# Kernel tuning notes

Hardware: AMD Instinct MI355X
Metric: run time of the kernel (lower is better)

The kernel has to match this reference:

```python
import jax, jax.numpy as jnp
import numpy as np

B, C, K, V, S = 16384, 1024, 128, 256, 6
HM, HG, M = 512, 384, 1024
LB = 2
GATE_DIM = C + K + 2 * V + 5  # 1669
CADENCE = 8.0
TEMP = 0.25
REFRESH_T, SPAWN_T, PROMOTE_T, RETIRE_T = 0.55, 0.60, 0.50, 0.15
DECAY = 0.995
EPS_N = 1e-6


def _mlp(x, W1, b1, W2, b2):
    return jax.nn.gelu(x @ W1 + b1, approximate=False) @ W2 + b2


def _l2norm(x):
    n = jnp.linalg.norm(x, axis=-1, keepdims=True)
    return x / jnp.maximum(n, EPS_N)


def setup_inputs():
    key = jax.random.key(0)
    ks = jax.random.split(key, 16)
    p = lambda k, sh: (0.02 * jax.random.normal(k, sh)).astype(jnp.float32)
    return {
        "context": jax.random.normal(ks[0], (B, C), jnp.float32),
        "ledger_bias": jax.random.normal(ks[1], (B, LB), jnp.float32),
        "keys": jax.random.normal(ks[2], (B, S, K), jnp.float32),
        "values": jax.random.normal(ks[3], (B, S, V), jnp.float32),
        "confidence": jax.random.uniform(ks[4], (B, S, 1), jnp.float32),
        "age": 16.0 * jax.random.uniform(ks[5], (B, S, 1), jnp.float32),
        "alive": (jax.random.uniform(ks[6], (B, S, 1)) > 0.3).astype(jnp.float32),
        "Wk1": p(ks[7], (C, HM)), "bk1": jnp.zeros(HM, jnp.float32),
        "Wk2": p(ks[8], (HM, K)), "bk2": jnp.zeros(K, jnp.float32),
        "Wv1": p(ks[9], (C, HM)), "bv1": jnp.zeros(HM, jnp.float32),
        "Wv2": p(ks[10], (HM, V)), "bv2": jnp.zeros(V, jnp.float32),
        "Wg1": p(ks[11], (4, GATE_DIM, HG)), "bg1": jnp.zeros((4, HG), jnp.float32),
        "Wg2": p(ks[12], (4, HG, 1)), "bg2": jnp.zeros((4, 1), jnp.float32),
        "Wsum": p(ks[13], (V, M)), "bsum": jnp.zeros(M, jnp.float32),
        "g_ln": jnp.ones(M, jnp.float32), "b_ln": jnp.zeros(M, jnp.float32),
    }


def _forward(context, ledger_bias, keys, values, confidence, age, alive,
             Wk1, bk1, Wk2, bk2, Wv1, bv1, Wv2, bv2,
             Wg1, bg1, Wg2, bg2, Wsum, bsum, g_ln, b_ln):
    cand_key = _l2norm(_mlp(context, Wk1, bk1, Wk2, bk2))   # [B,K]
    cand_val = _mlp(context, Wv1, bv1, Wv2, bv2)            # [B,V]
    # --- slot match: cosine similarity over live slots, gather best ---
    live = alive[..., 0] > 0                                # [B,S]
    safe_keys = _l2norm(keys + (1.0 - alive) * 1e-4)
    scores = jnp.einsum("bd,bsd->bs", cand_key, safe_keys)
    scores = jnp.where(live, scores, -1e4)
    has_live = jnp.any(live, axis=1, keepdims=True)         # [B,1]
    best_score = jnp.where(has_live, scores.max(axis=1, keepdims=True), 0.0)
    best_index = jnp.where(has_live, jnp.argmax(scores, axis=1, keepdims=True), 0)
    matched_val = jnp.take_along_axis(values, best_index[:, :, None], axis=1)[:, 0]
    matched_age = jnp.take_along_axis(age, best_index[:, :, None], axis=1)[:, 0]
    cadence_prior = jax.nn.sigmoid((matched_age - CADENCE) / CADENCE)
    surprise = 1.0 - best_score
    feats = jnp.concatenate([context, cand_key, cand_val, matched_val,
                             best_score, cadence_prior, surprise, ledger_bias], axis=-1)
    # --- four gate MLPs fused into one batched einsum ---
    h = jax.nn.gelu(jnp.einsum("bf,gfh->bgh", feats, Wg1) + bg1, approximate=False)
    probs = jax.nn.sigmoid(jnp.einsum("bgh,gho->bgo", h, Wg2) + bg2)[:, :, 0]  # [B,4]
    refresh_p, spawn_p, promote_p, retire_p = (probs[:, i:i + 1] for i in range(4))
    # --- soft masks (hard=False path) ---
    has_live_f = alive.max(axis=1)                          # [B,1]
    t = max(TEMP, 1e-4)
    refresh_raw = jax.nn.sigmoid((refresh_p - REFRESH_T) / t) * has_live_f
    spawn_raw = jax.nn.sigmoid((spawn_p - SPAWN_T) / t)
    denom = 1.0 + refresh_raw + spawn_raw
    refresh = refresh_raw / denom
    spawn = spawn_raw / denom
    promote = jax.nn.sigmoid((promote_p - PROMOTE_T) / t)
    retire = jax.nn.sigmoid((retire_p - RETIRE_T) / t)
    # --- spawn slot selection ---
    inactive = (alive[..., 0] < 0.5).astype(jnp.float32)
    has_inactive = inactive.max(axis=1, keepdims=True) > 0.5
    inactive_choice = jnp.argmax(inactive, axis=1, keepdims=True)
    utility = (confidence - 0.01 * age)[..., 0]
    utility = jnp.where(best_index == jnp.arange(S)[None, :], 1e4, utility)
    spawn_index = jnp.where(has_inactive, inactive_choice,
                            jnp.argmin(utility, axis=1, keepdims=True))
    # --- masked scatter update into slot memory ---
    match_hot = jax.nn.one_hot(best_index[:, 0], S, dtype=keys.dtype)[:, :, None]
    spawn_hot = jax.nn.one_hot(spawn_index[:, 0], S, dtype=keys.dtype)[:, :, None]
    refresh_slot = match_hot * refresh[:, None, :]
    spawn_slot = spawn_hot * spawn[:, None, :]
    retire_slot = match_hot * retire[:, None, :]
    write = jnp.clip(refresh_slot + spawn_slot, 0.0, 1.0)
    keys_n = keys * (1.0 - write) + write * cand_key[:, None, :]
    values_n = values * (1.0 - write) + write * cand_val[:, None, :]
    conf_n = (confidence * DECAY * (1.0 - write) + write) * (1.0 - retire_slot)
    age_n = (age + alive) * (1.0 - write)
    alive_n = jnp.clip(alive * (1.0 - retire_slot) + write, 0.0, 1.0)
    # --- confidence-weighted summary + promoted memory token ---
    w = alive_n * conf_n
    summary = (values_n * w).sum(axis=1) / (w.sum(axis=1) + EPS_N)  # [B,V]
    z = summary @ Wsum + bsum
    mu = z.mean(axis=-1, keepdims=True)
    var = ((z - mu) ** 2).mean(axis=-1, keepdims=True)
    promoted = promote * (((z - mu) / jnp.sqrt(var + 1e-5)) * g_ln + b_ln)
    return promoted, summary, keys_n, values_n, conf_n, age_n, alive_n


def reference(context, ledger_bias, keys, values, confidence, age, alive,
              Wk1, bk1, Wk2, bk2, Wv1, bv1, Wv2, bv2,
              Wg1, bg1, Wg2, bg2, Wsum, bsum, g_ln, b_ln):
    return _forward(context, ledger_bias, keys, values, confidence, age, alive,
                    Wk1, bk1, Wk2, bk2, Wv1, bv1, Wv2, bv2,
                    Wg1, bg1, Wg2, bg2, Wsum, bsum, g_ln, b_ln)
```

## Files before the change

### kernel.cpp

```cpp
#include <hip/hip_runtime.h>
#include <math.h>

static constexpr int Bsz  = 16384;
static constexpr int Cdim = 1024;
static constexpr int Kdim = 128;
static constexpr int Vdim = 256;
static constexpr int HMd  = 512;
static constexpr int GOUTd= 1536;
static constexpr int GDIM = 1669;
static constexpr int GPAD = 1728;
static constexpr int F2D  = 704;
static constexpr int Mdim = 1024;
static constexpr float TAU = 2e-3f;

typedef __attribute__((ext_vector_type(8))) _Float16 f16x8;
typedef __attribute__((ext_vector_type(4))) float f32x4;

__device__ __forceinline__ float sigm(float x){ return 1.0f/(1.0f+expf(-x)); }
__device__ __forceinline__ float gelu(float x){ return 0.5f*x*(1.0f+erff(x*0.70710678118654752440f)); }
__device__ __forceinline__ ushort f2h(float f){
    return __builtin_bit_cast(ushort, (_Float16)f);
}


__global__ __launch_bounds__(256) void k_zero(int* p){ if (threadIdx.x==0) *p = 0; }

__global__ __launch_bounds__(256) void k_cat(float* __restrict__ dst,
        const float* __restrict__ a, const float* __restrict__ b, int na, int ntot){
    int i = blockIdx.x*256 + threadIdx.x;
    if (i >= ntot) return;
    dst[i] = (i < na) ? a[i] : b[i-na];
}

__global__ __launch_bounds__(256) void k_wt(const float* __restrict__ W,
                                            ushort* __restrict__ Wt, int K, int N){
    __shared__ float tile[64][65];
    int n0 = blockIdx.x*64, k0 = blockIdx.y*64;
    int tx = threadIdx.x & 63, ty = threadIdx.x >> 6;
    #pragma unroll
    for (int i=0;i<64;i+=4)
        tile[ty+i][tx] = W[(size_t)(k0+ty+i)*N + n0 + tx];
    __syncthreads();
    #pragma unroll
    for (int i=0;i<64;i+=4)
        Wt[(size_t)(n0+ty+i)*K + k0 + tx] = f2h(tile[tx][ty+i]);
}

__global__ __launch_bounds__(256) void k_wg1t(const float* __restrict__ Wg1,
                                              ushort* __restrict__ Wt){
    __shared__ float tile[64][65];
    int g = blockIdx.z;
    int h0 = blockIdx.x*64, f0 = blockIdx.y*64;
    int tx = threadIdx.x & 63, ty = threadIdx.x >> 6;
    #pragma unroll
    for (int i=0;i<64;i+=4){
        int f = f0+ty+i;
        tile[ty+i][tx] = (f < GDIM) ? Wg1[((size_t)g*GDIM+f)*384 + h0+tx] : 0.0f;
    }
    __syncthreads();
    #pragma unroll
    for (int i=0;i<64;i+=4)
        Wt[((size_t)(g*384 + h0+ty+i))*GPAD + f0+tx] = f2h(tile[tx][ty+i]);
}

__global__ __launch_bounds__(256) void k_cvt(const float* __restrict__ x,
                                             ushort* __restrict__ y, size_t n4){
    size_t i = (size_t)blockIdx.x*256 + threadIdx.x;
    if (i >= n4) return;
    float4 v = ((const float4*)x)[i];
    ushort4 o = { f2h(v.x), f2h(v.y), f2h(v.z), f2h(v.w) };
    ((ushort4*)y)[i] = o;
}

__device__ __forceinline__ void gload_lds16(const void* g, void* l){
    typedef __attribute__((address_space(1))) const unsigned gu32;
    typedef __attribute__((address_space(3))) unsigned lu32;
    __builtin_amdgcn_global_load_lds((gu32*)(unsigned long long)g,
                                     (lu32*)(unsigned)(unsigned long long)l,
                                     16, 0, 0);
}

template<int ACT, int OUTM, int SRC, int NX>
__global__ __launch_bounds__(256) void k_mgemm(const ushort* __restrict__ A,
        const ushort* __restrict__ A2, const ushort* __restrict__ Bt,
        const float* __restrict__ bias, const float* __restrict__ Wg2,
        void* __restrict__ Cout, int K, int lda){
    __shared__ alignas(16) ushort lds[16384];
    ushort* As = lds;
    ushort* Bs = lds + 8192;
    int t = threadIdx.x;
    int l = t & 63, w = t >> 6;
    int wm = w >> 1, wn = w & 1;
    int nwg = NX * (int)gridDim.y;
    int orig = (int)blockIdx.y * NX + (int)blockIdx.x;
    int qq = nwg >> 3, rr = nwg & 7;
    int xcd = orig & 7, loc = orig >> 3;
    int wgid = (xcd < rr ? xcd*(qq+1) : rr*(qq+1) + (xcd-rr)*qq) + loc;
    int bx = wgid % NX;
    int by = wgid / NX;
    size_t row0 = (size_t)by * 128;
    int col0 = bx * 128;
    constexpr int N = NX*128;
    f32x4 acc[4][4] = {};
    int lrow = l >> 3;
    int lc8  = (l & 7) ^ lrow;

    for (int k0 = 0; k0 < K; k0 += 64){
        const ushort* Ag; int astr, koff;
        if (SRC == 1){
            if (k0 < 1024){ Ag = A;  astr = 1024; koff = k0; }
            else          { Ag = A2; astr = F2D;  koff = k0 - 1024; }
        } else if (SRC == 2){
            Ag = A; astr = lda; koff = k0 + (bx ? 512 : 0);
        } else { Ag = A; astr = lda; koff = k0; }
        #pragma unroll
        for (int i = 0; i < 4; ++i){
            int ch = w*4 + i;
            int r  = ch*8 + lrow;
            gload_lds16(Ag + (row0 + r)*(size_t)astr + koff + lc8*8, As + ch*512);
            gload_lds16(Bt + (size_t)(col0 + r)*K + k0 + lc8*8, Bs + ch*512);
        }
        __syncthreads();
        #pragma unroll
        for (int kk = 0; kk < 2; ++kk){
            f16x8 af[4], bfr[4];
            int j8 = kk*4 + (l >> 4);
            #pragma unroll
            for (int m = 0; m < 4; ++m){
                int row = wm*64 + m*16 + (l & 15);
                int c16 = j8 ^ (row & 7);
                af[m] = *(const f16x8*)(const void*)(As + row*64 + c16*8);
            }
            #pragma unroll
            for (int n = 0; n < 4; ++n){
                int rowb = wn*64 + n*16 + (l & 15);
                int c16 = j8 ^ (rowb & 7);
                bfr[n] = *(const f16x8*)(const void*)(Bs + rowb*64 + c16*8);
            }
            #pragma unroll
            for (int m = 0; m < 4; ++m)
                #pragma unroll
                for (int n = 0; n < 4; ++n)
                    acc[m][n] = __builtin_amdgcn_mfma_f32_16x16x32_f16(af[m], bfr[n], acc[m][n], 0, 0, 0);
        }
        __syncthreads();
    }
    int q = l >> 4, cf = l & 15;
    if (OUTM == 2){
        float* sacc = (float*)lds;
        if (t < 128) sacc[t] = 0.f;
        __syncthreads();
        #pragma unroll
        for (int m = 0; m < 4; ++m){
            #pragma unroll
            for (int i = 0; i < 4; ++i){
                float v = 0.f;
                #pragma unroll
                for (int n = 0; n < 4; ++n){
                    int col = col0 + wn*64 + n*16 + cf;
                    float z = acc[m][n][i] + bias[col];
                    v += gelu(z) * Wg2[col];
                }
                atomicAdd(&sacc[wm*64 + m*16 + q*4 + i], v);
            }
        }
        __syncthreads();
        if (t < 128) ((float*)Cout)[(row0 + t)*NX + bx] = sacc[t];
    } else {
        #pragma unroll
        for (int m = 0; m < 4; ++m){
            #pragma unroll
            for (int n = 0; n < 4; ++n){
                int col = col0 + wn*64 + n*16 + cf;
                float bv = bias[col];
                #pragma unroll
                for (int i = 0; i < 4; ++i){
                    size_t r = row0 + wm*64 + m*16 + q*4 + i;
                    float v = acc[m][n][i] + bv;
                    if (ACT == 1) v = gelu(v);
                    if (OUTM == 1) ((ushort*)Cout)[r*N + col] = f2h(v);
                    else           ((float*) Cout)[r*N + col] = v;
                }
            }
        }
    }
}

template<int ACT>
__global__ __launch_bounds__(256) void k_gemm_dyn(const float* __restrict__ A,
                                                  const float* __restrict__ W,
                                                  const float* __restrict__ bias,
                                                  float* __restrict__ C,
                                                  const int* __restrict__ cntp,
                                                  int N, int K){
    int M = (*cntp + 63) & ~63;
    size_t row0 = (size_t)blockIdx.y * 64;
    if ((int)row0 >= M) return;
    __shared__ float As[32][68];
    __shared__ float Ws[32][64];
    int t  = threadIdx.x;
    int tx = t & 15, ty = t >> 4;
    int col0 = blockIdx.x * 64;
    float acc[4][4] = {};
    int ra = t >> 3;
    int ca = (t & 7) << 2;
    int rw = t >> 4;
    int cw = (t & 15) << 2;
    for (int k0 = 0; k0 < K; k0 += 32){
        float4 a0 = *(const float4*)(A + (row0 + ra)*K + k0 + ca);
        float4 a1 = *(const float4*)(A + (row0 + ra + 32)*K + k0 + ca);
        float4 w0 = *(const float4*)(W + (size_t)(k0 + rw)*N + col0 + cw);
        float4 w1 = *(const float4*)(W + (size_t)(k0 + rw + 16)*N + col0 + cw);
        As[ca+0][ra] = a0.x; As[ca+1][ra] = a0.y; As[ca+2][ra] = a0.z; As[ca+3][ra] = a0.w;
        As[ca+0][ra+32] = a1.x; As[ca+1][ra+32] = a1.y; As[ca+2][ra+32] = a1.z; As[ca+3][ra+32] = a1.w;
        *(float4*)&Ws[rw][cw]    = w0;
        *(float4*)&Ws[rw+16][cw] = w1;
        __syncthreads();
        #pragma unroll
        for (int kk = 0; kk < 32; ++kk){
            float4 av = *(const float4*)&As[kk][ty*4];
            float4 wv = *(const float4*)&Ws[kk][tx*4];
            float a4[4] = {av.x, av.y, av.z, av.w};
            float w4[4] = {wv.x, wv.y, wv.z, wv.w};
            #pragma unroll
            for (int i=0;i<4;i++)
                #pragma unroll
                for (int j=0;j<4;j++)
                    acc[i][j] = fmaf(a4[i], w4[j], acc[i][j]);
        }
        __syncthreads();
    }
    #pragma unroll
    for (int i=0;i<4;i++){
        size_t r = row0 + ty*4 + i;
        #pragma unroll
        for (int j=0;j<4;j++){
            int c = col0 + tx*4 + j;
            float v = acc[i][j] + bias[c];
            if (ACT == 1) v = gelu(v);
            C[r*N + c] = v;
        }
    }
}

__global__ __launch_bounds__(256) void k_gather(const float* __restrict__ ctx,
        const int* __restrict__ flaglist, const int* __restrict__ flagcnt,
        float* __restrict__ fctx, int b0){
    int i = (blockIdx.x<<2) + (threadIdx.x>>6);
    int lane = threadIdx.x & 63;
    int cnt = *flagcnt;
    int cntpad = (cnt + 63) & ~63;
    if (i >= cntpad) return;
    float4* dst = (float4*)(fctx + (size_t)i*1024);
    if (i < cnt){
        const float4* src = (const float4*)(ctx + ((size_t)b0 + flaglist[i])*1024);
        #pragma unroll
        for (int j=0;j<4;j++) dst[lane + 64*j] = src[lane + 64*j];
    } else {
        float4 z = {0.f,0.f,0.f,0.f};
        #pragma unroll
        for (int j=0;j<4;j++) dst[lane + 64*j] = z;
    }
}

__global__ __launch_bounds__(256) void k_fixapply(const float* __restrict__ fck,
        const float* __restrict__ keys, const float* __restrict__ values,
        const float* __restrict__ age,  const float* __restrict__ alive,
        float* __restrict__ ckc, ushort* __restrict__ feats2, int* __restrict__ bidx,
        const int* __restrict__ flagcnt, const int* __restrict__ flaglist, int b0){
    int i = (blockIdx.x<<2) + (threadIdx.x>>6);
    int lane = threadIdx.x & 63;
    if (i >= *flagcnt) return;
    int w = flaglist[i];
    size_t b = (size_t)b0 + w;
    float2 c2 = ((const float2*)(fck + (size_t)i*128))[lane];
    float ss = c2.x*c2.x + c2.y*c2.y;
    #pragma unroll
    for (int o=32;o;o>>=1) ss += __shfl_xor(ss,o);
    float inv = 1.0f / fmaxf(sqrtf(ss), 1e-6f);
    float2 cc; cc.x = c2.x*inv; cc.y = c2.y*inv;
    ((float2*)(ckc + (size_t)w*128))[lane] = cc;
    ushort* f2 = feats2 + (size_t)w*F2D;
    { ushort2 o = { f2h(cc.x), f2h(cc.y) };
      ((ushort2*)f2)[lane] = o; }
    float s1v = -1e30f; int bi = 0; int anylive = 0;
    #pragma unroll
    for (int s=0;s<6;s++){
        float a = alive[b*6+s];
        float2 k2 = ((const float2*)(keys + (b*6+s)*128))[lane];
        float ks = k2.x*k2.x + k2.y*k2.y;
        float dt = cc.x*k2.x + cc.y*k2.y;
        #pragma unroll
        for (int o=32;o;o>>=1){ ks += __shfl_xor(ks,o); dt += __shfl_xor(dt,o); }
        float sc;
        if (a > 0.0f){ sc = dt / fmaxf(sqrtf(ks), 1e-6f); anylive = 1; }
        else sc = -1e4f;
        if (sc > s1v){ s1v = sc; bi = s; }
    }
    int bis = anylive ? bi : 0;
    float bsc = anylive ? s1v : 0.0f;
    float4 mv = ((const float4*)(values + (b*6+bis)*256))[lane];
    ushort4 mo = { f2h(mv.x), f2h(mv.y), f2h(mv.z), f2h(mv.w) };
    ((ushort4*)(f2+384))[lane] = mo;
    if (lane == 0){
        bidx[w] = bis;
        float mage = age[b*6 + bis];
        f2[640] = f2h(bsc);
        f2[641] = f2h(sigm((mage - 8.0f)*0.125f));
        f2[642] = f2h(1.0f - bsc);
    }
}

__global__ __launch_bounds__(256) void k_feats(
        const float* __restrict__ ledger, const float* __restrict__ keys,
        const float* __restrict__ values, const float* __restrict__ age,
        const float* __restrict__ alive,  const float* __restrict__ ckv,
        float* __restrict__ ckc, ushort* __restrict__ feats2,
        int* __restrict__ bidx, int* __restrict__ flagcnt, int* __restrict__ flaglist,
        int b0){
    int w = (blockIdx.x<<2) + (threadIdx.x>>6);
    int lane = threadIdx.x & 63;
    size_t b = (size_t)b0 + w;
    const float* ckr = ckv + (size_t)w*384;
    float2 cr2 = ((const float2*)ckr)[lane];
    float ssc = cr2.x*cr2.x + cr2.y*cr2.y;
    #pragma unroll
    for (int o=32;o;o>>=1) ssc += __shfl_xor(ssc,o);
    float invc = 1.0f / fmaxf(sqrtf(ssc), 1e-6f);
    float2 cc; cc.x = cr2.x*invc; cc.y = cr2.y*invc;
    ((float2*)(ckc + (size_t)w*128))[lane] = cc;
    float s1v = -1e30f, s2v = -1e30f; int bi = 0; int anylive = 0;
    #pragma unroll
    for (int s=0;s<6;s++){
        float a = alive[b*6+s];
        float2 k2 = ((const float2*)(keys + (b*6+s)*128))[lane];
        float ss = k2.x*k2.x + k2.y*k2.y;
        float dt = cc.x*k2.x + cc.y*k2.y;
        #pragma unroll
        for (int o=32;o;o>>=1){ ss += __shfl_xor(ss,o); dt += __shfl_xor(dt,o); }
        float sc;
        if (a > 0.0f){ sc = dt / fmaxf(sqrtf(ss), 1e-6f); anylive = 1; }
        else sc = -1e4f;
        if (sc > s1v){ s2v = s1v; s1v = sc; bi = s; }
        else if (sc > s2v) s2v = sc;
    }
    float best_score = anylive ? s1v : 0.0f;
    int bis = anylive ? bi : 0;
    if (lane == 0 && (s1v - s2v) < TAU){
        int pos = atomicAdd(flagcnt, 1);
        flaglist[pos] = w;
    }
    float4 mv = ((const float4*)(values + (b*6+bis)*256))[lane];
    float mage = age[b*6+bis];
    float cad = sigm((mage - 8.0f)*0.125f);
    ushort* f2 = feats2 + (size_t)w*F2D;
    { ushort2 o = { f2h(cc.x), f2h(cc.y) };
      ((ushort2*)f2)[lane] = o; }
    { float4 v = ((const float4*)(ckr+128))[lane];
      ushort4 o = { f2h(v.x), f2h(v.y), f2h(v.z), f2h(v.w) };
      ((ushort4*)(f2+128))[lane] = o; }
    { ushort4 o = { f2h(mv.x), f2h(mv.y), f2h(mv.z), f2h(mv.w) };
      ((ushort4*)(f2+384))[lane] = o; }
    if (lane == 0){
        f2[640] = f2h(best_score);
        f2[641] = f2h(cad);
        f2[642] = f2h(1.0f - best_score);
        f2[643] = f2h(ledger[b*2]);
        f2[644] = f2h(ledger[b*2+1]);
        bidx[w] = bis;
    }
    if (lane < GPAD - GDIM) f2[645+lane] = 0;
}

__global__ __launch_bounds__(256) void k_update(const float* __restrict__ keys,
        const float* __restrict__ values, const float* __restrict__ conf,
        const float* __restrict__ age,    const float* __restrict__ alive,
        const float* __restrict__ ckC,    const float* __restrict__ ckv,
        const float* __restrict__ part,   const float* __restrict__ bg2,
        const int* __restrict__ bidx,
        float* __restrict__ probsC,
        float* __restrict__ o_keys, float* __restrict__ o_vals,
        float* __restrict__ o_conf, float* __restrict__ o_age,
        float* __restrict__ o_aliv, float* __restrict__ o_sum,
        ushort* __restrict__ o_sumb, int b0){
    int w = (blockIdx.x<<2) + (threadIdx.x>>6);
    int lane = threadIdx.x & 63;
    size_t b = (size_t)b0 + w;
    const float* pp = part + (size_t)w*12;
    float pb[4];
    #pragma unroll
    for (int g=0; g<4; ++g)
        pb[g] = sigm(pp[3*g] + pp[3*g+1] + pp[3*g+2] + bg2[g]);
    if (lane < 4) probsC[w*4 + lane] = pb[lane];
    float rp = pb[0], sp = pb[1], tp = pb[3];
    float al[6], cf[6], ag[6];
    float hl = 0.f;
    #pragma unroll
    for (int s=0;s<6;s++){
        al[s]=alive[b*6+s]; cf[s]=conf[b*6+s]; ag[s]=age[b*6+s];
        hl = fmaxf(hl, al[s]);
    }
    float rr = hl * sigm((rp-0.55f)*4.0f);
    float sr = sigm((sp-0.60f)*4.0f);
    float den = 1.0f + rr + sr;
    float refresh = rr/den, spawn = sr/den;
    float retire = sigm((tp-0.15f)*4.0f);
    int bi = bidx[w];
    int ic = -1;
    #pragma unroll
    for (int s=5;s>=0;s--) if (al[s] < 0.5f) ic = s;
    int si;
    if (ic >= 0) si = ic;
    else {
        float bu = 1e30f; int am = 0;
        #pragma unroll
        for (int s=0;s<6;s++){
            float u = (s == bi) ? 1e4f : (cf[s] - 0.01f*ag[s]);
            if (u < bu){ bu = u; am = s; }
        }
        si = am;
    }
    float2 cc  = ((const float2*)(ckC + (size_t)w*128))[lane];
    float4 cvv = ((const float4*)(ckv + (size_t)w*384 + 128))[lane];
    float s0=0,s1=0,s2=0,s3=0, wsum=0;
    #pragma unroll
    for (int s=0;s<6;s++){
        float wr = refresh*(s==bi ? 1.0f:0.0f) + spawn*(s==si ? 1.0f:0.0f);
        wr = fminf(wr, 1.0f);
        float rs = (s==bi) ? retire : 0.0f;
        float om = 1.0f - wr;
        float2 k2 = ((const float2*)(keys + (b*6+s)*128))[lane];
        float2 kn; kn.x = k2.x*om + wr*cc.x; kn.y = k2.y*om + wr*cc.y;
        ((float2*)(o_keys + (b*6+s)*128))[lane] = kn;
        float4 vv = ((const float4*)(values + (b*6+s)*256))[lane];
        float4 vn;
        vn.x = vv.x*om + wr*cvv.x; vn.y = vv.y*om + wr*cvv.y;
        vn.z = vv.z*om + wr*cvv.z; vn.w = vv.w*om + wr*cvv.w;
        ((float4*)(o_vals + (b*6+s)*256))[lane] = vn;
        float cn  = (cf[s]*0.995f*om + wr) * (1.0f - rs);
        float an  = fminf(fmaxf(al[s]*(1.0f - rs) + wr, 0.0f), 1.0f);
        float agn = (ag[s] + al[s]) * om;
        float wgt = an * cn;
        wsum += wgt;
        s0 += vn.x*wgt; s1 += vn.y*wgt; s2 += vn.z*wgt; s3 += vn.w*wgt;
        if (lane == s){ o_conf[b*6+s] = cn; o_age[b*6+s] = agn; o_aliv[b*6+s] = an; }
    }
    float inv = 1.0f/(wsum + 1e-6f);
    float4 sm; sm.x = s0*inv; sm.y = s1*inv; sm.z = s2*inv; sm.w = s3*inv;
    ((float4*)(o_sum + b*256))[lane] = sm;
    ushort4 sb = { f2h(sm.x), f2h(sm.y), f2h(sm.z), f2h(sm.w) };
    ((ushort4*)(o_sumb + (size_t)w*256))[lane] = sb;
}

__global__ __launch_bounds__(256) void k_ln(const float* __restrict__ z,
        const float* __restrict__ probs, const float* __restrict__ g_ln,
        const float* __restrict__ b_ln,  float* __restrict__ o_prom, int b0){
    int w = blockIdx.x; int t = threadIdx.x;
    int lane = t & 63, wid = t >> 6;
    float4 v = ((const float4*)(z + (size_t)w*1024))[t];
    float s = v.x+v.y+v.z+v.w;
    #pragma unroll
    for (int o=32;o;o>>=1) s += __shfl_xor(s,o);
    __shared__ float red[4];
    if (lane==0) red[wid] = s;
    __syncthreads();
    float mu = (red[0]+red[1]+red[2]+red[3]) * (1.0f/1024.0f);
    float d0=v.x-mu, d1=v.y-mu, d2=v.z-mu, d3=v.w-mu;
    float ss = d0*d0+d1*d1+d2*d2+d3*d3;
    #pragma unroll
    for (int o=32;o;o>>=1) ss += __shfl_xor(ss,o);
    __syncthreads();
    if (lane==0) red[wid] = ss;
    __syncthreads();
    float var = (red[0]+red[1]+red[2]+red[3]) * (1.0f/1024.0f);
    float rstd = 1.0f / sqrtf(var + 1e-5f);
    float pm = sigm((probs[w*4+2]-0.50f)*4.0f);
    float4 g  = ((const float4*)g_ln)[t];
    float4 bb = ((const float4*)b_ln)[t];
    float4 o;
    o.x = pm*(d0*rstd*g.x + bb.x);
    o.y = pm*(d1*rstd*g.y + bb.y);
    o.z = pm*(d2*rstd*g.z + bb.z);
    o.w = pm*(d3*rstd*g.w + bb.w);
    ((float4*)(o_prom + ((size_t)b0 + w)*1024))[t] = o;
}

extern "C" void kernel_launch(void* const* d_in, const int* in_sizes, int n_in,
                              void* d_out, int out_size, void* d_ws, size_t ws_size,
                              hipStream_t stream){
    const float* ctx    = (const float*)d_in[0];
    const float* ledger = (const float*)d_in[1];
    const float* keys   = (const float*)d_in[2];
    const float* values = (const float*)d_in[3];
    const float* conf   = (const float*)d_in[4];
    const float* age    = (const float*)d_in[5];
    const float* alive  = (const float*)d_in[6];
    const float* Wk1 = (const float*)d_in[7];  const float* bk1 = (const float*)d_in[8];
    const float* Wk2 = (const float*)d_in[9];  const float* bk2 = (const float*)d_in[10];
    const float* Wv1 = (const float*)d_in[11]; const float* bv1 = (const float*)d_in[12];
    const float* Wv2 = (const float*)d_in[13]; const float* bv2 = (const float*)d_in[14];
    const float* Wg1 = (const float*)d_in[15]; const float* bg1 = (const float*)d_in[16];
    const float* Wg2 = (const float*)d_in[17]; const float* bg2 = (const float*)d_in[18];
    const float* Wsum= (const float*)d_in[19]; const float* bsum= (const float*)d_in[20];
    const float* g_ln= (const float*)d_in[21]; const float* b_ln= (const float*)d_in[22];

    float* out   = (float*)d_out;
    float* o_prom= out;
    float* o_sum = o_prom + (size_t)Bsz*Mdim;
    float* o_keys= o_sum  + (size_t)Bsz*Vdim;
    float* o_vals= o_keys + (size_t)Bsz*6*Kdim;
    float* o_conf= o_vals + (size_t)Bsz*6*Vdim;
    float* o_age = o_conf + (size_t)Bsz*6;
    float* o_aliv= o_age  + (size_t)Bsz*6;

    char* p = (char*)d_ws;
    auto alloc = [&](size_t bytes)->char*{
        char* r = p; p += (bytes + 255) & ~(size_t)255; return r;
    };
    ushort* ctxh  = (ushort*)alloc((size_t)Bsz*Cdim*2);
    ushort* W1m   = (ushort*)alloc((size_t)1024*Cdim*2);
    ushort* W2m   = (ushort*)alloc((size_t)384*HMd*2);
    ushort* Wg1tt = (ushort*)alloc((size_t)GOUTd*GPAD*2);
    ushort* Wsumt = (ushort*)alloc((size_t)Mdim*Vdim*2);
    float*  biasm1= (float*) alloc(1024*4);
    float*  biasm2= (float*) alloc(384*4);
    size_t fixed = (size_t)(p - (char*)d_ws);
    size_t per_row = 2048  + 1536  + 512  + 1408
                   + 48  + 4096  + 512  + 16
                   + 4 + 4 + 2048  + 512  + 128 ;
    int CB = 16384;
    while (CB > 128 && fixed + (size_t)CB*per_row + 16384 > ws_size) CB >>= 1;
    ushort* H      = (ushort*)alloc((size_t)CB*1024*2);
    float*  ckv    = (float*) alloc((size_t)CB*384*4);
    float*  ckc    = (float*) alloc((size_t)CB*Kdim*4);
    ushort* feats2 = (ushort*)alloc((size_t)CB*F2D*2);
    float*  part   = (float*) alloc((size_t)CB*12*4);
    float*  zbuf   = (float*) alloc((size_t)CB*Mdim*4);
    ushort* sumb   = (ushort*)alloc((size_t)CB*Vdim*2);
    float*  probsC = (float*) alloc((size_t)CB*4*4);
    int*    bidxC  = (int*)   alloc((size_t)CB*4);
    int*    flagl  = (int*)   alloc((size_t)CB*4);
    int*    flagc  = (int*)   alloc(256);
    float*  fH     = (float*) alloc((size_t)CB*HMd*4);
    float*  fck    = (float*) alloc((size_t)CB*Kdim*4);
    float*  fctx   = zbuf;

    dim3 blk(256);
    k_cvt<<<(int)(((size_t)Bsz*Cdim/4 + 255)/256), blk, 0, stream>>>(ctx, ctxh, (size_t)Bsz*Cdim/4);
    k_wt<<<dim3(HMd/64,  Cdim/64), blk, 0, stream>>>(Wk1, W1m,             Cdim, HMd);
    k_wt<<<dim3(HMd/64,  Cdim/64), blk, 0, stream>>>(Wv1, W1m + 512*Cdim,  Cdim, HMd);
    k_wt<<<dim3(Kdim/64, HMd/64),  blk, 0, stream>>>(Wk2, W2m,             HMd, Kdim);
    k_wt<<<dim3(Vdim/64, HMd/64),  blk, 0, stream>>>(Wv2, W2m + 128*HMd,   HMd, Vdim);
    k_wt<<<dim3(Mdim/64, Vdim/64), blk, 0, stream>>>(Wsum, Wsumt, Vdim, Mdim);
    k_wg1t<<<dim3(384/64, GPAD/64, 4), blk, 0, stream>>>(Wg1, Wg1tt);
    k_cat<<<(1024+255)/256, blk, 0, stream>>>(biasm1, bk1, bv1, 512, 1024);
    k_cat<<<(384+255)/256,  blk, 0, stream>>>(biasm2, bk2, bv2, 128, 384);

    for (int b0 = 0; b0 < Bsz; b0 += CB){
        k_zero<<<1, blk, 0, stream>>>(flagc);
        k_mgemm<1,1,0,8><<<dim3(8, CB/128), blk, 0, stream>>>(
            ctxh + (size_t)b0*Cdim, nullptr, W1m, biasm1, nullptr, H, Cdim, Cdim);
        k_mgemm<0,0,2,3><<<dim3(3, CB/128), blk, 0, stream>>>(
            H, nullptr, W2m, biasm2, nullptr, ckv, HMd, 1024);
        k_feats<<<CB/4, blk, 0, stream>>>(ledger, keys, values, age, alive,
                                          ckv, ckc, feats2, bidxC, flagc, flagl, b0);
        k_gather<<<CB/4, blk, 0, stream>>>(ctx, flagl, flagc, fctx, b0);
        k_gemm_dyn<1><<<dim3(HMd/64,  CB/64), blk, 0, stream>>>(fctx, Wk1, bk1, fH,  flagc, HMd,  Cdim);
        k_gemm_dyn<0><<<dim3(Kdim/64, CB/64), blk, 0, stream>>>(fH,   Wk2, bk2, fck, flagc, Kdim, HMd);
        k_fixapply<<<CB/4, blk, 0, stream>>>(fck, keys, values, age, alive,
                                             ckc, feats2, bidxC, flagc, flagl, b0);
        k_mgemm<0,2,1,12><<<dim3(12, CB/128), blk, 0, stream>>>(
            ctxh + (size_t)b0*Cdim, feats2, Wg1tt, bg1, Wg2, part, GPAD, 0);
        k_update<<<CB/4, blk, 0, stream>>>(keys, values, conf, age, alive, ckc, ckv,
                                           part, bg2, bidxC, probsC,
                                           o_keys, o_vals, o_conf, o_age, o_aliv,
                                           o_sum, sumb, b0);
        k_mgemm<0,0,0,8><<<dim3(8, CB/128), blk, 0, stream>>>(
            sumb, nullptr, Wsumt, bsum, nullptr, zbuf, Vdim, Vdim);
        k_ln<<<CB, blk, 0, stream>>>(zbuf, probsC, g_ln, b_ln, o_prom, b0);
    }
}
```

Measured before the change: 498.7 us.

## Double-buffer GEMM LDS loads, use fast GELU/sigmoid, store LN input as fp16

The MFMA GEMM now double-buffers its LDS tiles, issuing the next tile's global-to-LDS loads before computing on the current one, with explicit vmcnt waits and barriers. The erf-based GELU is replaced by an Abramowitz-Stegun polynomial using hardware reciprocal and fast exp, and sigmoid uses __expf. The summary projection GEMM writes fp16 output, which layer norm reads back, halving that intermediate's traffic. These add approximation error in GELU and in the pre-layernorm activations, and double the LDS footprint per block, which may lower occupancy.

```diff
diff --git a/kernel.cpp b/kernel.cpp
--- a/kernel.cpp
+++ b/kernel.cpp
@@ -14,10 +14,21 @@
 static constexpr float TAU = 2e-3f;
 
 typedef __attribute__((ext_vector_type(8))) _Float16 f16x8;
+typedef __attribute__((ext_vector_type(4))) _Float16 f16x4;
 typedef __attribute__((ext_vector_type(4))) float f32x4;
 
-__device__ __forceinline__ float sigm(float x){ return 1.0f/(1.0f+expf(-x)); }
-__device__ __forceinline__ float gelu(float x){ return 0.5f*x*(1.0f+erff(x*0.70710678118654752440f)); }
+__device__ __forceinline__ float sigm(float x){ return 1.0f/(1.0f+__expf(-x)); }
+__device__ __forceinline__ float gelu(float x){
+    float y = 0.70710678118654752440f * x;
+    float a = fabsf(y);
+    float t1 = __builtin_amdgcn_rcpf(fmaf(0.3275911f, a, 1.0f));
+    float p = t1*fmaf(t1, fmaf(t1, fmaf(t1, fmaf(t1, 1.061405429f, -1.453152027f),
+                                         1.421413741f), -0.284496736f), 0.254829592f);
+    float e = __expf(-a*a);
+    float er = fmaf(-p, e, 1.0f);
+    er = (y < 0.0f) ? -er : er;
+    return 0.5f*x*(1.0f+er);
+}
 __device__ __forceinline__ ushort f2h(float f){
     return __builtin_bit_cast(ushort, (_Float16)f);
 }
@@ -85,9 +96,7 @@
         const ushort* __restrict__ A2, const ushort* __restrict__ Bt,
         const float* __restrict__ bias, const float* __restrict__ Wg2,
         void* __restrict__ Cout, int K, int lda){
-    __shared__ alignas(16) ushort lds[16384];
-    ushort* As = lds;
-    ushort* Bs = lds + 8192;
+    __shared__ alignas(16) ushort lds[32768];
     int t = threadIdx.x;
     int l = t & 63, w = t >> 6;
     int wm = w >> 1, wn = w & 1;
@@ -104,15 +113,18 @@
     f32x4 acc[4][4] = {};
     int lrow = l >> 3;
     int lc8  = (l & 7) ^ lrow;
-
-    for (int k0 = 0; k0 < K; k0 += 64){
-        const ushort* Ag; int astr, koff;
+    int nt = K >> 6;
+
+    auto stage = [&](int buf, int k0){
+        const ushort* Ag; int astr; int koff;
         if (SRC == 1){
             if (k0 < 1024){ Ag = A;  astr = 1024; koff = k0; }
             else          { Ag = A2; astr = F2D;  koff = k0 - 1024; }
         } else if (SRC == 2){
             Ag = A; astr = lda; koff = k0 + (bx ? 512 : 0);
         } else { Ag = A; astr = lda; koff = k0; }
+        ushort* As = lds + buf*16384;
+        ushort* Bs = As + 8192;
         #pragma unroll
         for (int i = 0; i < 4; ++i){
             int ch = w*4 + i;
@@ -120,7 +132,10 @@
             gload_lds16(Ag + (row0 + r)*(size_t)astr + koff + lc8*8, As + ch*512);
             gload_lds16(Bt + (size_t)(col0 + r)*K + k0 + lc8*8, Bs + ch*512);
         }
-        __syncthreads();
+    };
+    auto compute = [&](int buf){
+        const ushort* As = lds + buf*16384;
+        const ushort* Bs = As + 8192;
         #pragma unroll
         for (int kk = 0; kk < 2; ++kk){
             f16x8 af[4], bfr[4];
@@ -143,10 +158,23 @@
                 for (int n = 0; n < 4; ++n)
                     acc[m][n] = __builtin_amdgcn_mfma_f32_16x16x32_f16(af[m], bfr[n], acc[m][n], 0, 0, 0);
         }
-        __syncthreads();
-    }
+    };
+
+    stage(0, 0);
+    for (int tt = 0; tt < nt-1; ++tt){
+        __builtin_amdgcn_s_barrier();
+        stage((tt+1)&1, (tt+1)<<6);
+        asm volatile("s_waitcnt vmcnt(8)" ::: "memory");
+        __builtin_amdgcn_s_barrier();
+        compute(tt&1);
+    }
+    asm volatile("s_waitcnt vmcnt(0)" ::: "memory");
+    __builtin_amdgcn_s_barrier();
+    compute((nt-1)&1);
+
     int q = l >> 4, cf = l & 15;
     if (OUTM == 2){
+        __syncthreads();
         float* sacc = (float*)lds;
         if (t < 128) sacc[t] = 0.f;
         __syncthreads();
@@ -452,20 +480,21 @@
     ((ushort4*)(o_sumb + (size_t)w*256))[lane] = sb;
 }
 
-__global__ __launch_bounds__(256) void k_ln(const float* __restrict__ z,
+__global__ __launch_bounds__(256) void k_ln(const ushort* __restrict__ z,
         const float* __restrict__ probs, const float* __restrict__ g_ln,
         const float* __restrict__ b_ln,  float* __restrict__ o_prom, int b0){
     int w = blockIdx.x; int t = threadIdx.x;
     int lane = t & 63, wid = t >> 6;
-    float4 v = ((const float4*)(z + (size_t)w*1024))[t];
-    float s = v.x+v.y+v.z+v.w;
+    f16x4 hv = ((const f16x4*)(z + (size_t)w*1024))[t];
+    float v0 = (float)hv[0], v1 = (float)hv[1], v2 = (float)hv[2], v3 = (float)hv[3];
+    float s = v0+v1+v2+v3;
     #pragma unroll
     for (int o=32;o;o>>=1) s += __shfl_xor(s,o);
     __shared__ float red[4];
     if (lane==0) red[wid] = s;
     __syncthreads();
     float mu = (red[0]+red[1]+red[2]+red[3]) * (1.0f/1024.0f);
-    float d0=v.x-mu, d1=v.y-mu, d2=v.z-mu, d3=v.w-mu;
+    float d0=v0-mu, d1=v1-mu, d2=v2-mu, d3=v3-mu;
     float ss = d0*d0+d1*d1+d2*d2+d3*d3;
     #pragma unroll
     for (int o=32;o;o>>=1) ss += __shfl_xor(ss,o);
@@ -544,6 +573,7 @@
     float*  fH     = (float*) alloc((size_t)CB*HMd*4);
     float*  fck    = (float*) alloc((size_t)CB*Kdim*4);
     float*  fctx   = zbuf;
+    ushort* zh     = (ushort*)zbuf;
 
     dim3 blk(256);
     k_cvt<<<(int)(((size_t)Bsz*Cdim/4 + 255)/256), blk, 0, stream>>>(ctx, ctxh, (size_t)Bsz*Cdim/4);
@@ -575,8 +605,8 @@
                                            part, bg2, bidxC, probsC,
                                            o_keys, o_vals, o_conf, o_age, o_aliv,
                                            o_sum, sumb, b0);
-        k_mgemm<0,0,0,8><<<dim3(8, CB/128), blk, 0, stream>>>(
-            sumb, nullptr, Wsumt, bsum, nullptr, zbuf, Vdim, Vdim);
-        k_ln<<<CB, blk, 0, stream>>>(zbuf, probsC, g_ln, b_ln, o_prom, b0);
-    }
-}
+        k_mgemm<0,1,0,8><<<dim3(8, CB/128), blk, 0, stream>>>(
+            sumb, nullptr, Wsumt, bsum, nullptr, zh, Vdim, Vdim);
+        k_ln<<<CB, blk, 0, stream>>>(zh, probsC, g_ln, b_ln, o_prom, b0);
+    }
+}
```

Result: faster. 471.3 us (-5.5%).
